# Kernel tuning notes

Measured on AMD Instinct MI355X. Metric: run time of the kernel, lower is better.

The kernel has to match this reference:

```python
import jax, jax.numpy as jnp
import numpy as np

B, N_Z, N_E, D = 16, 2048, 2048, 512

def setup_inputs() -> dict:
    key = jax.random.key(0)
    kz, ke, km = jax.random.split(key, 3)
    z = jax.random.normal(kz, (B, N_Z, D), dtype=jnp.float32)
    e = jax.random.normal(ke, (B, N_E, D), dtype=jnp.float32)
    M = jax.random.normal(km, (D, D), dtype=jnp.float32)  # init: normal(0, 1)
    return {"z": z, "e": e, "M": M}

def reference(z, e, M):
    # a = z @ M @ e^T : [B, Nz, Ne]
    zM = jnp.einsum('bnd,de->bne', z, M)
    a = jnp.einsum('bnd,bmd->bnm', zM, e)
    a = jax.nn.sigmoid(a)
    # softmax over dim=1 (the Nz axis), as in the torch code
    A = jax.nn.softmax(a, axis=1)
    # out = A @ e : [B, Nz, D]
    return jnp.einsum('bnm,bmd->bnd', A, e)
```

## Files before the change

kernel.cpp:

```cpp
#include <hip/hip_runtime.h>
#include <hip/hip_bf16.h>
#include <stdint.h>

#define BB 16
#define NZ 2048
#define NE 2048
#define DD 512

typedef unsigned short u16;
typedef __attribute__((ext_vector_type(8))) _Float16 f16x8;
typedef __attribute__((ext_vector_type(4))) float f32x4;

__device__ __forceinline__ u16 f2h(float f) {
  _Float16 h = (_Float16)f;
  return __builtin_bit_cast(u16, h);
}

__device__ __forceinline__ float h2f(u16 h) {
  return (float)__builtin_bit_cast(_Float16, h);
}

__device__ __forceinline__ void gload_lds16(const void* g, void* l) {
  auto gp = (const __attribute__((address_space(1))) uint32_t*)g;
  auto lp = (__attribute__((address_space(3))) uint32_t*)l;
  __builtin_amdgcn_global_load_lds(gp, lp, 16, 0, 0);
}

__global__ void k_cvt(const float* __restrict__ in, u16* __restrict__ out, int n4) {
  int i = blockIdx.x * blockDim.x + threadIdx.x;
  int stride = gridDim.x * blockDim.x;
  for (; i < n4; i += stride) {
    float4 v = ((const float4*)in)[i];
    ushort4 o;
    o.x = f2h(v.x); o.y = f2h(v.y); o.z = f2h(v.z); o.w = f2h(v.w);
    ((ushort4*)out)[i] = o;
  }
}

__global__ void k_mt(const float* __restrict__ M, u16* __restrict__ Mt) {
  __shared__ float t[32][33];
  int bx = blockIdx.x * 32;
  int by = blockIdx.y * 32;
  for (int r = 0; r < 32; r += 8)
    t[threadIdx.y + r][threadIdx.x] = M[(size_t)(by + threadIdx.y + r) * DD + bx + threadIdx.x];
  __syncthreads();
  for (int r = 0; r < 32; r += 8)
    Mt[(size_t)(bx + threadIdx.y + r) * DD + by + threadIdx.x] = f2h(t[threadIdx.x][threadIdx.y + r]);
}

__global__ void k_et(const u16* __restrict__ eH, const float* __restrict__ cs,
                     u16* __restrict__ eT) {
  __shared__ float t[32][33];
  int b = blockIdx.z;
  int m0 = blockIdx.y * 32, d0 = blockIdx.x * 32;
  const u16* eb = eH + (size_t)b * NE * DD;
  const float* csb = cs + (size_t)b * NE;
  for (int r = 0; r < 32; r += 8) {
    int m = m0 + threadIdx.y + r;
    t[threadIdx.y + r][threadIdx.x] =
        h2f(eb[(size_t)m * DD + d0 + threadIdx.x]) * (2048.0f / csb[m]);
  }
  __syncthreads();
  u16* eTb = eT + (size_t)b * DD * NE;
  for (int r = 0; r < 32; r += 8) {
    int d = d0 + threadIdx.y + r;
    eTb[(size_t)d * NE + m0 + threadIdx.x] = f2h(t[threadIdx.x][threadIdx.y + r]);
  }
}

template<int EPI, int KDIM>
__global__ __launch_bounds__(256, 3) void k_gemm(
    const u16* __restrict__ A, const u16* __restrict__ Bt, void* __restrict__ Cp,
    int Ndim, long long sAb, long long sBb, long long sCb,
    float* __restrict__ colsum, int csld)
{
  extern __shared__ char lds[];
  constexpr int NT = KDIM / 32;

  const int gx = gridDim.x, gy = gridDim.y;
  const int nwg = gx * gy * gridDim.z;
  const int hid = blockIdx.x + gx * (blockIdx.y + gy * blockIdx.z);
  const int logical = (hid & 7) * (nwg >> 3) + (hid >> 3);
  const int bx = logical % gx;
  const int rem0 = logical / gx;
  const int by = rem0 % gy;
  const int bz = rem0 / gy;

  const int tid = threadIdx.x;
  const int lane = tid & 63;
  const int wid = tid >> 6;
  const int wr = wid >> 1;
  const int wc = wid & 1;

  const int row0 = by * 128;
  const int col0 = bx * 128;

  const u16* Ab = A + (long long)bz * sAb;
  const u16* Bb = Bt + (long long)bz * sBb;

  const u16* srcA[2]; const u16* srcB[2];
#pragma unroll
  for (int c = 0; c < 2; ++c) {
    int idx = c * 256 + tid;
    int r = idx >> 2;
    int cL = idx & 3;
    int q = cL ^ ((r >> 1) & 3);
    srcA[c] = Ab + (long long)(row0 + r) * KDIM + q * 8;
    srcB[c] = Bb + (long long)(col0 + r) * KDIM + q * 8;
  }

  auto stage = [&](char* dA, char* dB, int k0) {
#pragma unroll
    for (int c = 0; c < 2; ++c)
      gload_lds16(srcA[c] + k0, dA + (c * 256 + wid * 64) * 16);
#pragma unroll
    for (int c = 0; c < 2; ++c)
      gload_lds16(srcB[c] + k0, dB + (c * 256 + wid * 64) * 16);
  };

  f32x4 acc[4][4] = {};

  const int p15 = lane & 15;
  const int cswz = (lane >> 4) ^ ((p15 >> 1) & 3);

  stage(lds, lds + 16384, 0);
  __syncthreads();

  for (int t = 0; t < NT; ++t) {
    const int buf = t & 1;
    char* lA = lds + buf * 8192;
    char* lB = lds + 16384 + buf * 8192;
    if (t + 1 < NT)
      stage(lds + (buf ^ 1) * 8192, lds + 16384 + (buf ^ 1) * 8192, (t + 1) * 32);

    f16x8 af[4], bf[4];
#pragma unroll
    for (int m = 0; m < 4; ++m) {
      int r = wr * 64 + m * 16 + p15;
      af[m] = *(const f16x8*)(lA + r * 64 + cswz * 16);
    }
#pragma unroll
    for (int n = 0; n < 4; ++n) {
      int r = wc * 64 + n * 16 + p15;
      bf[n] = *(const f16x8*)(lB + r * 64 + cswz * 16);
    }
#pragma unroll
    for (int m = 0; m < 4; ++m)
#pragma unroll
      for (int n = 0; n < 4; ++n)
        acc[m][n] = __builtin_amdgcn_mfma_f32_16x16x32_f16(af[m], bf[n], acc[m][n], 0, 0, 0);

    __syncthreads();
  }

  const int rr = (lane >> 4) * 4;
  const int cc = lane & 15;
  const int grow = row0 + wr * 64;
  const int gcol = col0 + wc * 64;

  if constexpr (EPI == 0 || EPI == 1) {
    char* wb = lds + wid * 8192;
    float csum[4] = {0.f, 0.f, 0.f, 0.f};
#pragma unroll
    for (int m = 0; m < 4; ++m)
#pragma unroll
      for (int n = 0; n < 4; ++n)
#pragma unroll
        for (int j = 0; j < 4; ++j) {
          float x = acc[m][n][j];
          float v;
          if constexpr (EPI == 1) {
            float s = 1.f / (1.f + __expf(-x));
            v = __expf(s);
            csum[n] += v;
          } else {
            v = x;
          }
          int rl = m * 16 + rr + j;
          int col = n * 16 + cc;
          int chunk = (col >> 3) ^ (rl & 7);
          *(u16*)(wb + rl * 128 + chunk * 16 + ((col * 2) & 15)) = f2h(v);
        }
    if constexpr (EPI == 1) {
#pragma unroll
      for (int n = 0; n < 4; ++n) {
        float v = csum[n];
        v += __shfl_xor(v, 16, 64);
        v += __shfl_xor(v, 32, 64);
        if ((lane >> 4) == 0)
          atomicAdd(&colsum[(long long)bz * csld + gcol + n * 16 + cc], v);
      }
    }
    __syncthreads();
    u16* C = (u16*)Cp + (long long)bz * sCb;
#pragma unroll
    for (int s = 0; s < 8; ++s) {
      int rl = (lane >> 3) + s * 8;
      int chunk = (lane & 7) ^ (rl & 7);
      f16x8 v = *(const f16x8*)(wb + rl * 128 + chunk * 16);
      *(f16x8*)(&C[(long long)(grow + rl) * Ndim + gcol + (lane & 7) * 8]) = v;
    }
  } else {
    float* C = (float*)Cp + (long long)bz * sCb;
    char* wb = lds + wid * 8192;
#pragma unroll
    for (int h = 0; h < 2; ++h) {
      if (h) __syncthreads();
#pragma unroll
      for (int mm = 0; mm < 2; ++mm) {
        int m = h * 2 + mm;
#pragma unroll
        for (int n = 0; n < 4; ++n)
#pragma unroll
          for (int j = 0; j < 4; ++j) {
            int rl = mm * 16 + rr + j;
            int col = n * 16 + cc;
            int chunk = (col >> 2) ^ (rl & 15);
            *(float*)(wb + rl * 256 + chunk * 16 + ((col * 4) & 15)) =
                acc[m][n][j] * (1.0f / 2048.0f);
          }
      }
      __syncthreads();
#pragma unroll
      for (int s = 0; s < 8; ++s) {
        int rl = (lane >> 4) + s * 4;
        int chunk = (lane & 15) ^ (rl & 15);
        f32x4 v = *(const f32x4*)(wb + rl * 256 + chunk * 16);
        *(f32x4*)(&C[(long long)(grow + h * 32 + rl) * Ndim + gcol + (lane & 15) * 4]) = v;
      }
    }
  }
}

extern "C" void kernel_launch(void* const* d_in, const int* in_sizes, int n_in,
                              void* d_out, int out_size, void* d_ws, size_t ws_size,
                              hipStream_t stream) {
  const float* z = (const float*)d_in[0];
  const float* e = (const float*)d_in[1];
  const float* M = (const float*)d_in[2];
  float* out = (float*)d_out;
  char* ws = (char*)d_ws;

  u16* S    = (u16*)(ws + 0LL);
  u16* zM   = (u16*)(ws + 134217728LL);
  u16* zH   = (u16*)(ws + 167772160LL);
  u16* eH   = (u16*)(ws + 201326592LL);
  u16* Mt   = (u16*)(ws + 234881024LL);
  float* cs = (float*)(ws + 235405312LL);

  hipMemsetAsync(cs, 0, (size_t)BB * NE * sizeof(float), stream);

  k_cvt<<<4096, 256, 0, stream>>>(z, zH, BB * NZ * DD / 4);
  k_cvt<<<4096, 256, 0, stream>>>(e, eH, BB * NE * DD / 4);
  k_mt<<<dim3(16, 16), dim3(32, 8), 0, stream>>>(M, Mt);

  k_gemm<0, 512><<<dim3(DD / 128, (BB * NZ) / 128, 1), 256, 32768, stream>>>(
      zH, Mt, zM, DD, 0LL, 0LL, 0LL, nullptr, 0);

  k_gemm<1, 512><<<dim3(NE / 128, NZ / 128, BB), 256, 32768, stream>>>(
      zM, eH, S, NE,
      (long long)NZ * DD, (long long)NE * DD, (long long)NZ * NE, cs, NE);

  u16* eT = zH;
  k_et<<<dim3(DD / 32, NE / 32, BB), dim3(32, 8), 0, stream>>>(eH, cs, eT);

  k_gemm<2, 2048><<<dim3(DD / 128, NZ / 128, BB), 256, 32768, stream>>>(
      S, eT, out, DD,
      (long long)NZ * NE, (long long)DD * NE, (long long)NZ * DD, nullptr, 0);
}
```

Baseline: 305.1 us.

## Triple-buffer GEMM LDS pipeline and vectorize conversion and transpose kernels

The GEMM main loop moves from double to triple buffering with prefetch distance two. It uses explicit vmcnt waits and raw barriers so global-to-LDS loads overlap MFMA work longer. The fp32-to-fp16 conversion now handles 8 elements per thread with 16-byte stores. The scaled transpose of e uses 64x64 tiles with 16-byte loads and stores and an XOR-swizzled LDS layout. LDS per block rises from 32 KB to 48 KB, which may reduce how many blocks fit per CU under the 3-block launch bound.

```diff
diff --git a/kernel.cpp b/kernel.cpp
--- a/kernel.cpp
+++ b/kernel.cpp
@@ -9,6 +9,7 @@
 
 typedef unsigned short u16;
 typedef __attribute__((ext_vector_type(8))) _Float16 f16x8;
+typedef __attribute__((ext_vector_type(8))) short s16x8;
 typedef __attribute__((ext_vector_type(4))) float f32x4;
 
 __device__ __forceinline__ u16 f2h(float f) {
@@ -26,14 +27,22 @@
   __builtin_amdgcn_global_load_lds(gp, lp, 16, 0, 0);
 }
 
-__global__ void k_cvt(const float* __restrict__ in, u16* __restrict__ out, int n4) {
+#define FENCE() asm volatile("" ::: "memory")
+#define BARRIER() do { FENCE(); __builtin_amdgcn_s_barrier(); FENCE(); } while (0)
+#define WAIT_VM(n) asm volatile("s_waitcnt vmcnt(" #n ")" ::: "memory")
+
+__global__ void k_cvt(const float* __restrict__ in, u16* __restrict__ out, int n8) {
   int i = blockIdx.x * blockDim.x + threadIdx.x;
   int stride = gridDim.x * blockDim.x;
-  for (; i < n4; i += stride) {
-    float4 v = ((const float4*)in)[i];
-    ushort4 o;
-    o.x = f2h(v.x); o.y = f2h(v.y); o.z = f2h(v.z); o.w = f2h(v.w);
-    ((ushort4*)out)[i] = o;
+  for (; i < n8; i += stride) {
+    float4 v0 = ((const float4*)in)[i * 2];
+    float4 v1 = ((const float4*)in)[i * 2 + 1];
+    s16x8 o;
+    o[0] = (short)f2h(v0.x); o[1] = (short)f2h(v0.y);
+    o[2] = (short)f2h(v0.z); o[3] = (short)f2h(v0.w);
+    o[4] = (short)f2h(v1.x); o[5] = (short)f2h(v1.y);
+    o[6] = (short)f2h(v1.z); o[7] = (short)f2h(v1.w);
+    ((s16x8*)out)[i] = o;
   }
 }
 
@@ -50,21 +59,38 @@
 
 __global__ void k_et(const u16* __restrict__ eH, const float* __restrict__ cs,
                      u16* __restrict__ eT) {
-  __shared__ float t[32][33];
-  int b = blockIdx.z;
-  int m0 = blockIdx.y * 32, d0 = blockIdx.x * 32;
+  __shared__ u16 sm[64 * 72];
+  const int t = threadIdx.x;
+  const int b = blockIdx.z;
+  const int d0 = blockIdx.x * 64;
+  const int m0 = blockIdx.y * 64;
   const u16* eb = eH + (size_t)b * NE * DD;
   const float* csb = cs + (size_t)b * NE;
-  for (int r = 0; r < 32; r += 8) {
-    int m = m0 + threadIdx.y + r;
-    t[threadIdx.y + r][threadIdx.x] =
-        h2f(eb[(size_t)m * DD + d0 + threadIdx.x]) * (2048.0f / csb[m]);
+#pragma unroll
+  for (int it = 0; it < 2; ++it) {
+    int idx = it * 256 + t;
+    int ml = idx >> 3;
+    int dc = idx & 7;
+    s16x8 v = *(const s16x8*)(eb + (size_t)(m0 + ml) * DD + d0 + dc * 8);
+    float sc = 2048.0f / csb[m0 + ml];
+    int bl = ml >> 3, il = ml & 7;
+#pragma unroll
+    for (int j = 0; j < 8; ++j) {
+      int d = dc * 8 + j;
+      int pc = ((bl ^ j) << 3) + il;
+      sm[d * 72 + pc] = f2h(h2f((u16)v[j]) * sc);
+    }
   }
   __syncthreads();
   u16* eTb = eT + (size_t)b * DD * NE;
-  for (int r = 0; r < 32; r += 8) {
-    int d = d0 + threadIdx.y + r;
-    eTb[(size_t)d * NE + m0 + threadIdx.x] = f2h(t[threadIdx.x][threadIdx.y + r]);
+#pragma unroll
+  for (int it = 0; it < 2; ++it) {
+    int idx = it * 256 + t;
+    int dl = idx >> 3;
+    int mc = idx & 7;
+    int pb = mc ^ (dl & 7);
+    s16x8 v = *(const s16x8*)&sm[dl * 72 + pb * 8];
+    *(s16x8*)(eTb + (size_t)(d0 + dl) * NE + m0 + mc * 8) = v;
   }
 }
 
@@ -109,40 +135,43 @@
     srcB[c] = Bb + (long long)(col0 + r) * KDIM + q * 8;
   }
 
-  auto stage = [&](char* dA, char* dB, int k0) {
+  auto stage = [&](int t) {
+    const int k0 = t * 32;
+    char* d = lds + (t % 3) * 16384;
 #pragma unroll
     for (int c = 0; c < 2; ++c)
-      gload_lds16(srcA[c] + k0, dA + (c * 256 + wid * 64) * 16);
+      gload_lds16(srcA[c] + k0, d + (c * 256 + wid * 64) * 16);
 #pragma unroll
     for (int c = 0; c < 2; ++c)
-      gload_lds16(srcB[c] + k0, dB + (c * 256 + wid * 64) * 16);
+      gload_lds16(srcB[c] + k0, d + 8192 + (c * 256 + wid * 64) * 16);
   };
-
-  f32x4 acc[4][4] = {};
 
   const int p15 = lane & 15;
   const int cswz = (lane >> 4) ^ ((p15 >> 1) & 3);
 
-  stage(lds, lds + 16384, 0);
-  __syncthreads();
+  f32x4 acc[4][4] = {};
+
+  stage(0);
+  stage(1);
+  WAIT_VM(4);
+  BARRIER();
 
   for (int t = 0; t < NT; ++t) {
-    const int buf = t & 1;
-    char* lA = lds + buf * 8192;
-    char* lB = lds + 16384 + buf * 8192;
-    if (t + 1 < NT)
-      stage(lds + (buf ^ 1) * 8192, lds + 16384 + (buf ^ 1) * 8192, (t + 1) * 32);
+    char* lA = lds + (t % 3) * 16384;
+    char* lB = lA + 8192;
 
     f16x8 af[4], bf[4];
 #pragma unroll
     for (int m = 0; m < 4; ++m) {
       int r = wr * 64 + m * 16 + p15;
-      af[m] = *(const f16x8*)(lA + r * 64 + cswz * 16);
+      int c4 = (lane >> 4) ^ ((r >> 1) & 3);
+      af[m] = *(const f16x8*)(lA + r * 64 + c4 * 16);
     }
 #pragma unroll
     for (int n = 0; n < 4; ++n) {
       int r = wc * 64 + n * 16 + p15;
-      bf[n] = *(const f16x8*)(lB + r * 64 + cswz * 16);
+      int c4 = (lane >> 4) ^ ((r >> 1) & 3);
+      bf[n] = *(const f16x8*)(lB + r * 64 + c4 * 16);
     }
 #pragma unroll
     for (int m = 0; m < 4; ++m)
@@ -150,13 +179,21 @@
       for (int n = 0; n < 4; ++n)
         acc[m][n] = __builtin_amdgcn_mfma_f32_16x16x32_f16(af[m], bf[n], acc[m][n], 0, 0, 0);
 
-    __syncthreads();
-  }
+    BARRIER();
+    if (t + 2 < NT) stage(t + 2);
+    if (t + 1 < NT) {
+      if (t + 2 < NT) { WAIT_VM(4); } else { WAIT_VM(0); }
+      BARRIER();
+    }
+  }
+
+  __syncthreads();
 
   const int rr = (lane >> 4) * 4;
   const int cc = lane & 15;
   const int grow = row0 + wr * 64;
   const int gcol = col0 + wc * 64;
+  (void)cswz;
 
   if constexpr (EPI == 0 || EPI == 1) {
     char* wb = lds + wid * 8192;
@@ -250,21 +287,21 @@
 
   hipMemsetAsync(cs, 0, (size_t)BB * NE * sizeof(float), stream);
 
-  k_cvt<<<4096, 256, 0, stream>>>(z, zH, BB * NZ * DD / 4);
-  k_cvt<<<4096, 256, 0, stream>>>(e, eH, BB * NE * DD / 4);
+  k_cvt<<<4096, 256, 0, stream>>>(z, zH, BB * NZ * DD / 8);
+  k_cvt<<<4096, 256, 0, stream>>>(e, eH, BB * NE * DD / 8);
   k_mt<<<dim3(16, 16), dim3(32, 8), 0, stream>>>(M, Mt);
 
-  k_gemm<0, 512><<<dim3(DD / 128, (BB * NZ) / 128, 1), 256, 32768, stream>>>(
+  k_gemm<0, 512><<<dim3(DD / 128, (BB * NZ) / 128, 1), 256, 49152, stream>>>(
       zH, Mt, zM, DD, 0LL, 0LL, 0LL, nullptr, 0);
 
-  k_gemm<1, 512><<<dim3(NE / 128, NZ / 128, BB), 256, 32768, stream>>>(
+  k_gemm<1, 512><<<dim3(NE / 128, NZ / 128, BB), 256, 49152, stream>>>(
       zM, eH, S, NE,
       (long long)NZ * DD, (long long)NE * DD, (long long)NZ * NE, cs, NE);
 
   u16* eT = zH;
-  k_et<<<dim3(DD / 32, NE / 32, BB), dim3(32, 8), 0, stream>>>(eH, cs, eT);
-
-  k_gemm<2, 2048><<<dim3(DD / 128, NZ / 128, BB), 256, 32768, stream>>>(
+  k_et<<<dim3(DD / 64, NE / 64, BB), 256, 0, stream>>>(eH, cs, eT);
+
+  k_gemm<2, 2048><<<dim3(DD / 128, NZ / 128, BB), 256, 49152, stream>>>(
       S, eT, out, DD,
       (long long)NZ * NE, (long long)DD * NE, (long long)NZ * DD, nullptr, 0);
 }
```

Measured after the change: 277.6 us. 9.0% less time.
